# Kernel optimization log

Measured on AMD Instinct MI355X. Metric: run time of the kernel, lower is better.

The kernel has to match this reference:

```python
import jax, jax.numpy as jnp
import numpy as np
from jax import lax

B, S, F, D, H, L, A = 16, 512, 64, 512, 8, 4, 3
E = D // H  # head_dim = 64

def _gelu(t):
    return jax.nn.gelu(t, approximate=False)  # torch nn.GELU() is exact erf

def _make_masks():
    i = jnp.arange(S)[:, None]
    j = jnp.arange(S)[None, :]
    d = jnp.abs(i - j)
    ms = []
    for h in range(min(5, H)):
        dil = 2 ** h
        ms.append((d <= dil) | (d % (2 ** (h + 1)) == 0))
    m = jnp.stack(ms)  # [5,S,S] bool
    idx = jnp.minimum(jnp.arange(H), m.shape[0] - 1)
    return m[idx]  # [H,S,S]

MASKS = _make_masks()

def _ln(x, g, b, eps=1e-5):
    mu = jnp.mean(x, -1, keepdims=True)
    var = jnp.mean((x - mu) ** 2, -1, keepdims=True)
    return (x - mu) * lax.rsqrt(var + eps) * g + b

def _conv1d(x_ncw, w, b):
    y = lax.conv_general_dilated(x_ncw, w, (1,), [(1, 1)],
                                 dimension_numbers=("NCH", "OIH", "NCH"))
    return y + b[None, :, None]

def _attn(x, Wq, bq, Wk, bk, Wv, bv, Wo, bo):
    # x: [B,S,D]; Wq/Wk/Wv: [H,E,D] (stacked per-head Linear weights)
    q = jnp.einsum("bsd,hed->bhse", x, Wq) + bq[None, :, None, :]
    k = jnp.einsum("bsd,hed->bhse", x, Wk) + bk[None, :, None, :]
    v = jnp.einsum("bsd,hed->bhse", x, Wv) + bv[None, :, None, :]
    s = jnp.einsum("bhse,bhte->bhst", q, k) / (E ** 0.5)
    s = jnp.where(MASKS[None], s, -jnp.inf)  # log-sparse masked_fill
    p = jax.nn.softmax(s, axis=-1)
    o = jnp.einsum("bhst,bhte->bhse", p, v)
    o = o.transpose(0, 2, 1, 3).reshape(x.shape[0], x.shape[1], D)  # concat heads
    return o @ Wo.T + bo

def _forward(x, conv1_w, conv1_b, conv2_w, conv2_b, emb_w, emb_b, pos,
             Wq, bq, Wk, bk, Wv, bv, Wo, bo, ln1_g, ln1_b, ln2_g, ln2_b,
             W1, b1, W2, b2, lnf_g, lnf_b,
             a1_w, a1_b, a2_w, a2_b, a3_w, a3_b, a4_w, a4_b,
             c1_w, c1_b, c2_w, c2_b, c3_w, c3_b, c4_w, c4_b):
    # feature extractor: two conv1d+GELU over time axis
    h0 = _gelu(_conv1d(x.transpose(0, 2, 1), conv1_w, conv1_b))
    h0 = _gelu(_conv1d(h0, conv2_w, conv2_b)).transpose(0, 2, 1)  # [B,S,D]
    z = h0 @ emb_w.T + emb_b + pos[:, :S]  # input embedding + positional
    for l in range(L):  # PyraFormer blocks (pre-norm residual)
        z = z + _attn(_ln(z, ln1_g[l], ln1_b[l]),
                      Wq[l], bq[l], Wk[l], bk[l], Wv[l], bv[l], Wo[l], bo[l])
        h = _ln(z, ln2_g[l], ln2_b[l])
        z = z + (_gelu(h @ W1[l].T + b1[l]) @ W2[l].T + b2[l])
    z = _ln(z, lnf_g, lnf_b)
    feat = z[:, -1, :]  # last timestep features

    def head(f, layers):
        (w1, bb1), (w2, bb2), (w3, bb3), (w4, bb4) = layers
        f = _gelu(f @ w1.T + bb1)
        f = _gelu(f @ w2.T + bb2)
        f = _gelu(f @ w3.T + bb3)
        return f @ w4.T + bb4

    policy = head(feat, [(a1_w, a1_b), (a2_w, a2_b), (a3_w, a3_b), (a4_w, a4_b)])
    value = head(feat, [(c1_w, c1_b), (c2_w, c2_b), (c3_w, c3_b), (c4_w, c4_b)])
    return policy, value

def setup_inputs() -> dict:
    key = jax.random.key(0)
    ks = iter(jax.random.split(key, 64))
    r = lambda shape, s=0.05: jax.random.normal(next(ks), shape, jnp.float32) * s
    return {
        "x": jax.random.normal(next(ks), (B, S, F), jnp.float32),
        "conv1_w": r((D // 2, F, 3)), "conv1_b": jnp.zeros((D // 2,)),
        "conv2_w": r((D, D // 2, 3)), "conv2_b": jnp.zeros((D,)),
        "emb_w": r((D, D)), "emb_b": jnp.zeros((D,)),
        "pos": r((1, S, D), 0.02),
        "Wq": r((L, H, E, D)), "bq": jnp.zeros((L, H, E)),
        "Wk": r((L, H, E, D)), "bk": jnp.zeros((L, H, E)),
        "Wv": r((L, H, E, D)), "bv": jnp.zeros((L, H, E)),
        "Wo": r((L, D, D)), "bo": jnp.zeros((L, D)),
        "ln1_g": jnp.ones((L, D)), "ln1_b": jnp.zeros((L, D)),
        "ln2_g": jnp.ones((L, D)), "ln2_b": jnp.zeros((L, D)),
        "W1": r((L, 4 * D, D)), "b1": jnp.zeros((L, 4 * D)),
        "W2": r((L, D, 4 * D)), "b2": jnp.zeros((L, D)),
        "lnf_g": jnp.ones((D,)), "lnf_b": jnp.zeros((D,)),
        "a1_w": r((128, D)), "a1_b": jnp.zeros((128,)),
        "a2_w": r((256, 128)), "a2_b": jnp.zeros((256,)),
        "a3_w": r((57, 256)), "a3_b": jnp.zeros((57,)),
        "a4_w": r((A, 57)), "a4_b": jnp.zeros((A,)),
        "c1_w": r((128, D)), "c1_b": jnp.zeros((128,)),
        "c2_w": r((256, 128)), "c2_b": jnp.zeros((256,)),
        "c3_w": r((57, 256)), "c3_b": jnp.zeros((57,)),
        "c4_w": r((1, 57)), "c4_b": jnp.zeros((1,)),
    }

def reference(x, conv1_w, conv1_b, conv2_w, conv2_b, emb_w, emb_b, pos,
              Wq, bq, Wk, bk, Wv, bv, Wo, bo, ln1_g, ln1_b, ln2_g, ln2_b,
              W1, b1, W2, b2, lnf_g, lnf_b,
              a1_w, a1_b, a2_w, a2_b, a3_w, a3_b, a4_w, a4_b,
              c1_w, c1_b, c2_w, c2_b, c3_w, c3_b, c4_w, c4_b):
    return _forward(x, conv1_w, conv1_b, conv2_w, conv2_b, emb_w, emb_b, pos,
                    Wq, bq, Wk, bk, Wv, bv, Wo, bo, ln1_g, ln1_b, ln2_g, ln2_b,
                    W1, b1, W2, b2, lnf_g, lnf_b,
                    a1_w, a1_b, a2_w, a2_b, a3_w, a3_b, a4_w, a4_b,
                    c1_w, c1_b, c2_w, c2_b, c3_w, c3_b, c4_w, c4_b)
```

## Files before the change

### kernel.cpp

```cpp
#include <hip/hip_runtime.h>
#include <hip/hip_bf16.h>
#include <cstdint>

typedef __attribute__((ext_vector_type(8))) short bf16x8;
typedef __attribute__((ext_vector_type(4))) float f32x4;
typedef unsigned short u16;

#define DEV __device__ __forceinline__

DEV float b2f(u16 u) {
  union { unsigned int i; float f; } v; v.i = ((unsigned int)u) << 16; return v.f;
}
DEV u16 f2b(float f) {
  __hip_bfloat16 h = __float2bfloat16(f);
  return *reinterpret_cast<u16*>(&h);
}
DEV float erf_fast(float x) {
  float ax = fabsf(x);
  float t = __builtin_amdgcn_rcpf(fmaf(0.3275911f, ax, 1.0f));
  float p = t * fmaf(t, fmaf(t, fmaf(t, fmaf(t, 1.061405429f, -1.453152027f),
                                     1.421413741f), -0.284496736f), 0.254829592f);
  float r = fmaf(-p, __expf(-ax * ax), 1.0f);
  return copysignf(r, x);
}
DEV float gelu_f(float x) { return 0.5f * x * (1.0f + erf_fast(x * 0.70710678118654752f)); }

DEV void async_cp16(const u16* g, u16* l) {
  __builtin_amdgcn_global_load_lds(
      (const __attribute__((address_space(1))) void*)g,
      (__attribute__((address_space(3))) void*)l, 16, 0, 0);
}

__global__ void probe_kernel(const unsigned int* __restrict__ g, int* __restrict__ flag) {
  if (threadIdx.x == 0 && blockIdx.x == 0) *flag = (*g == 0x3F800000u) ? 1 : 0;
}

struct CvtArgs {
  const void* src[42];
  unsigned int off[43];
};

struct alignas(16) U8v { u16 u[8]; };
struct alignas(8)  U4v { u16 u[4]; };

__global__ __launch_bounds__(256) void cvt_kernel(CvtArgs a, int n_t, unsigned int total,
                                                  const int* __restrict__ flag,
                                                  u16* __restrict__ dst) {
  unsigned int i8 = (blockIdx.x * 256u + threadIdx.x) * 8u;
  if (i8 >= total) return;
  int t = 0;
  while (t + 1 < n_t && i8 >= a.off[t + 1]) t++;
  unsigned int j = i8 - a.off[t];
  bool in_seg = (i8 + 8 <= a.off[t + 1]) && (i8 + 8 <= total);
  int fp32 = *flag;
  if (fp32) {
    if (in_seg && ((j & 3) == 0)) {
      const float* s = (const float*)a.src[t] + j;
      float4 v0 = *(const float4*)s;
      float4 v1 = *(const float4*)(s + 4);
      U8v o;
      o.u[0] = f2b(v0.x); o.u[1] = f2b(v0.y); o.u[2] = f2b(v0.z); o.u[3] = f2b(v0.w);
      o.u[4] = f2b(v1.x); o.u[5] = f2b(v1.y); o.u[6] = f2b(v1.z); o.u[7] = f2b(v1.w);
      *(U8v*)(dst + i8) = o;
    } else {
      for (int k = 0; k < 8; k++) {
        unsigned int i = i8 + k;
        if (i >= total) break;
        int tt = t;
        while (tt + 1 < n_t && i >= a.off[tt + 1]) tt++;
        dst[i] = f2b(((const float*)a.src[tt])[i - a.off[tt]]);
      }
    }
  } else {
    if (in_seg && ((j & 7) == 0)) {
      *(U8v*)(dst + i8) = *(const U8v*)((const u16*)a.src[t] + j);
    } else {
      for (int k = 0; k < 8; k++) {
        unsigned int i = i8 + k;
        if (i >= total) break;
        int tt = t;
        while (tt + 1 < n_t && i >= a.off[tt + 1]) tt++;
        dst[i] = ((const u16*)a.src[tt])[i - a.off[tt]];
      }
    }
  }
}

__global__ __launch_bounds__(256) void gemm_bt44(
    const u16* __restrict__ A, const u16* __restrict__ W,
    const u16* __restrict__ bias,
    u16* __restrict__ outB, float* __restrict__ outF,
    int N, int K, int mode)
{
  __shared__ __align__(16) u16 As[2][64 * 32];
  __shared__ __align__(16) u16 Bs[2][64 * 32];
  int t = threadIdx.x, l = t & 63, w = t >> 6;
  int wr = w >> 1, wc = w & 1;
  int col = l & 15, quad = l >> 4;
  int q8 = (quad ^ ((col >> 1) & 3)) * 8;
  int m0 = blockIdx.x * 64;
  int n0 = blockIdx.y * 64;

  f32x4 acc[2][2];
#pragma unroll
  for (int i = 0; i < 2; i++)
#pragma unroll
    for (int j = 0; j < 2; j++) acc[i][j] = (f32x4){0.f, 0.f, 0.f, 0.f};

  int ra = t >> 2;
  int ca = (t & 3) ^ ((ra >> 1) & 3);
  const u16* a1 = A + (size_t)(m0 + ra) * K + ca * 8;
  const u16* b1 = W + (size_t)(n0 + ra) * K + ca * 8;

  int nK = K >> 5;
  async_cp16(a1, &As[0][t * 8]);
  async_cp16(b1, &Bs[0][t * 8]);
  for (int ki = 0; ki < nK; ki++) {
    int cur = ki & 1;
    if (ki + 1 < nK) {
      int nxt = cur ^ 1, kt = (ki + 1) << 5;
      async_cp16(a1 + kt, &As[nxt][t * 8]);
      async_cp16(b1 + kt, &Bs[nxt][t * 8]);
      __builtin_amdgcn_s_waitcnt(0x0F72);
    } else {
      __builtin_amdgcn_s_waitcnt(0x0F70);
    }
    __builtin_amdgcn_s_barrier();
    __builtin_amdgcn_sched_barrier(0);
    bf16x8 af[2], bfv[2];
#pragma unroll
    for (int mi = 0; mi < 2; mi++)
      af[mi] = *(const bf16x8*)&As[cur][(wr * 32 + mi * 16 + col) * 32 + q8];
#pragma unroll
    for (int ni = 0; ni < 2; ni++)
      bfv[ni] = *(const bf16x8*)&Bs[cur][(wc * 32 + ni * 16 + col) * 32 + q8];
#pragma unroll
    for (int mi = 0; mi < 2; mi++)
#pragma unroll
      for (int ni = 0; ni < 2; ni++)
        acc[mi][ni] = __builtin_amdgcn_mfma_f32_16x16x32_bf16(bfv[ni], af[mi], acc[mi][ni], 0, 0, 0);
    __builtin_amdgcn_sched_barrier(0);
    __builtin_amdgcn_s_barrier();
  }

  int mBase = m0 + wr * 32, nBase = n0 + wc * 32;
  if (mode == 1) {
#pragma unroll
    for (int mi = 0; mi < 2; mi++) {
      int m = mBase + mi * 16 + col;
      size_t rowOff = (size_t)m * N;
#pragma unroll
      for (int ni = 0; ni < 2; ni++) {
        int n4 = nBase + ni * 16 + quad * 4;
        U4v bb = *(const U4v*)&bias[n4];
        f32x4 v = acc[mi][ni];
        U4v o;
#pragma unroll
        for (int r = 0; r < 4; r++) o.u[r] = f2b(gelu_f(v[r] + b2f(bb.u[r])));
        *(U4v*)&outB[rowOff + n4] = o;
      }
    }
  } else {
#pragma unroll
    for (int mi = 0; mi < 2; mi++) {
      int m = mBase + mi * 16 + col;
      size_t rowOff = (size_t)m * N;
#pragma unroll
      for (int ni = 0; ni < 2; ni++) {
        int n4 = nBase + ni * 16 + quad * 4;
        U4v bb = *(const U4v*)&bias[n4];
        f32x4 v = acc[mi][ni];
        float4* p = (float4*)&outF[rowOff + n4];
        float4 zv = *p;
        zv.x += v[0] + b2f(bb.u[0]);
        zv.y += v[1] + b2f(bb.u[1]);
        zv.z += v[2] + b2f(bb.u[2]);
        zv.w += v[3] + b2f(bb.u[3]);
        *p = zv;
      }
    }
  }
}

__global__ __launch_bounds__(256) void gemm_qkv64(
    const u16* __restrict__ A,
    const u16* __restrict__ Wq, const u16* __restrict__ Wk, const u16* __restrict__ Wv,
    const u16* __restrict__ bq, const u16* __restrict__ bk, const u16* __restrict__ bv,
    u16* __restrict__ outQ, u16* __restrict__ outK, u16* __restrict__ outVT, int K)
{
  __shared__ __align__(16) u16 As[2][64 * 32];
  __shared__ __align__(16) u16 Bs[2][128 * 32];
  int t = threadIdx.x, l = t & 63, w = t >> 6;
  int wr = w >> 1, wc = w & 1;
  int col = l & 15, quad = l >> 4;
  int q8 = (quad ^ ((col >> 1) & 3)) * 8;
  int m0 = blockIdx.x * 64;
  int sel = blockIdx.y >> 2;
  int n0 = (blockIdx.y & 3) * 128;
  const u16* W = sel == 0 ? Wq : (sel == 1 ? Wk : Wv);
  const u16* bias = sel == 0 ? bq : (sel == 1 ? bk : bv);
  const bool swp = (sel < 2);
  const float scl = sel == 0 ? 0.125f : 1.0f;

  f32x4 acc[2][4];
#pragma unroll
  for (int i = 0; i < 2; i++)
#pragma unroll
    for (int j = 0; j < 4; j++) acc[i][j] = (f32x4){0.f, 0.f, 0.f, 0.f};

  int ra = t >> 2;
  int ca = (t & 3) ^ ((ra >> 1) & 3);
  int g1i = t, g2i = t + 256;
  int rb1 = g1i >> 2, rb2 = g2i >> 2;
  int cb1 = (g1i & 3) ^ ((rb1 >> 1) & 3);
  int cb2 = (g2i & 3) ^ ((rb2 >> 1) & 3);
  const u16* a1 = A + (size_t)(m0 + ra) * K + ca * 8;
  const u16* b1 = W + (size_t)(n0 + rb1) * K + cb1 * 8;
  const u16* b2 = W + (size_t)(n0 + rb2) * K + cb2 * 8;

  int nK = K >> 5;
  async_cp16(a1, &As[0][t * 8]);
  async_cp16(b1, &Bs[0][g1i * 8]);
  async_cp16(b2, &Bs[0][g2i * 8]);
  for (int ki = 0; ki < nK; ki++) {
    int cur = ki & 1;
    if (ki + 1 < nK) {
      int nxt = cur ^ 1, kt = (ki + 1) << 5;
      async_cp16(a1 + kt, &As[nxt][t * 8]);
      async_cp16(b1 + kt, &Bs[nxt][g1i * 8]);
      async_cp16(b2 + kt, &Bs[nxt][g2i * 8]);
      __builtin_amdgcn_s_waitcnt(0x0F73);
    } else {
      __builtin_amdgcn_s_waitcnt(0x0F70);
    }
    __builtin_amdgcn_s_barrier();
    __builtin_amdgcn_sched_barrier(0);
    bf16x8 af[2], bfv[4];
#pragma unroll
    for (int mi = 0; mi < 2; mi++)
      af[mi] = *(const bf16x8*)&As[cur][(wr * 32 + mi * 16 + col) * 32 + q8];
#pragma unroll
    for (int ni = 0; ni < 4; ni++)
      bfv[ni] = *(const bf16x8*)&Bs[cur][(wc * 64 + ni * 16 + col) * 32 + q8];
    if (swp) {
#pragma unroll
      for (int mi = 0; mi < 2; mi++)
#pragma unroll
        for (int ni = 0; ni < 4; ni++)
          acc[mi][ni] = __builtin_amdgcn_mfma_f32_16x16x32_bf16(bfv[ni], af[mi], acc[mi][ni], 0, 0, 0);
    } else {
#pragma unroll
      for (int mi = 0; mi < 2; mi++)
#pragma unroll
        for (int ni = 0; ni < 4; ni++)
          acc[mi][ni] = __builtin_amdgcn_mfma_f32_16x16x32_bf16(af[mi], bfv[ni], acc[mi][ni], 0, 0, 0);
    }
    __builtin_amdgcn_sched_barrier(0);
    __builtin_amdgcn_s_barrier();
  }

  int mBase = m0 + wr * 32, nBase = n0 + wc * 64;
  if (swp) {
    u16* outB = sel == 0 ? outQ : outK;
#pragma unroll
    for (int mi = 0; mi < 2; mi++) {
      int m = mBase + mi * 16 + col;
      size_t rowOff = (size_t)m * 512;
#pragma unroll
      for (int ni = 0; ni < 4; ni++) {
        int n4 = nBase + ni * 16 + quad * 4;
        U4v bb = *(const U4v*)&bias[n4];
        f32x4 v = acc[mi][ni];
        U4v o;
#pragma unroll
        for (int r = 0; r < 4; r++) o.u[r] = f2b((v[r] + b2f(bb.u[r])) * scl);
        *(U4v*)&outB[rowOff + n4] = o;
      }
    }
  } else {
    int b = m0 >> 9;
    int sB = m0 & 511;
#pragma unroll
    for (int mi = 0; mi < 2; mi++) {
      int s4 = sB + wr * 32 + mi * 16 + quad * 4;
#pragma unroll
      for (int ni = 0; ni < 4; ni++) {
        int n = nBase + ni * 16 + col;
        int h = n >> 6, e = n & 63;
        float bvv = b2f(bias[n]);
        f32x4 v = acc[mi][ni];
        U4v o;
#pragma unroll
        for (int r = 0; r < 4; r++) o.u[r] = f2b(v[r] + bvv);
        *(U4v*)&outVT[((size_t)((b * 8 + h) * 64 + e)) * 512 + s4] = o;
      }
    }
  }
}

__global__ __launch_bounds__(256) void zinit_kernel(const u16* __restrict__ pos,
                                                    float* __restrict__ z)
{
  int i = (blockIdx.x * 256 + threadIdx.x) * 8;
  int n = i & 511;
  int m = i >> 9;
  int s = m & 511;
  U8v p = *(const U8v*)&pos[s * 512 + n];
  float4 o0 = {b2f(p.u[0]), b2f(p.u[1]), b2f(p.u[2]), b2f(p.u[3])};
  float4 o1 = {b2f(p.u[4]), b2f(p.u[5]), b2f(p.u[6]), b2f(p.u[7])};
  *(float4*)(z + i) = o0;
  *(float4*)(z + i + 4) = o1;
}

__global__ void im2col3_kernel(const u16* __restrict__ src,
                               u16* __restrict__ dst, int C)
{
  int m = blockIdx.x;
  int k = blockIdx.y * blockDim.x + threadIdx.x;
  int ci = k / 3;
  int tap = k - ci * 3;
  int s = m & 511;
  int sp = s + tap - 1;
  u16 val = 0;
  if (sp >= 0 && sp < 512) val = src[(size_t)(m + tap - 1) * C + ci];
  dst[(size_t)m * (3 * C) + k] = val;
}

__global__ __launch_bounds__(256) void ln_kernel(
    const float* __restrict__ z, const u16* __restrict__ gam,
    const u16* __restrict__ bet, u16* __restrict__ out)
{
  int w = threadIdx.x >> 6, l = threadIdx.x & 63;
  int row = blockIdx.x * 4 + w;
  const float* zr = z + (size_t)row * 512;
  float4 v0 = *(const float4*)(zr + l * 8);
  float4 v1 = *(const float4*)(zr + l * 8 + 4);
  float x[8] = {v0.x, v0.y, v0.z, v0.w, v1.x, v1.y, v1.z, v1.w};
  float s = 0.f;
#pragma unroll
  for (int i = 0; i < 8; i++) s += x[i];
#pragma unroll
  for (int mm = 1; mm < 64; mm <<= 1) s += __shfl_xor(s, mm, 64);
  float mu = s * (1.0f / 512.0f);
  float vs = 0.f;
#pragma unroll
  for (int i = 0; i < 8; i++) { float d = x[i] - mu; vs += d * d; }
#pragma unroll
  for (int mm = 1; mm < 64; mm <<= 1) vs += __shfl_xor(vs, mm, 64);
  float rs = rsqrtf(vs * (1.0f / 512.0f) + 1e-5f);
  U8v gg = *(const U8v*)(gam + l * 8);
  U8v bb = *(const U8v*)(bet + l * 8);
  U8v o;
#pragma unroll
  for (int i = 0; i < 8; i++) o.u[i] = f2b((x[i] - mu) * rs * b2f(gg.u[i]) + b2f(bb.u[i]));
  *(U8v*)(out + (size_t)row * 512 + l * 8) = o;
}

__global__ __launch_bounds__(256) void lnf_kernel(
    const float* __restrict__ z, const u16* __restrict__ gam,
    const u16* __restrict__ bet, u16* __restrict__ feat)
{
  int w = threadIdx.x >> 6, l = threadIdx.x & 63;
  int b = blockIdx.x * 4 + w;
  const float* zr = z + ((size_t)b * 512 + 511) * 512;
  float4 v0 = *(const float4*)(zr + l * 8);
  float4 v1 = *(const float4*)(zr + l * 8 + 4);
  float x[8] = {v0.x, v0.y, v0.z, v0.w, v1.x, v1.y, v1.z, v1.w};
  float s = 0.f;
#pragma unroll
  for (int i = 0; i < 8; i++) s += x[i];
#pragma unroll
  for (int mm = 1; mm < 64; mm <<= 1) s += __shfl_xor(s, mm, 64);
  float mu = s * (1.0f / 512.0f);
  float vs = 0.f;
#pragma unroll
  for (int i = 0; i < 8; i++) { float d = x[i] - mu; vs += d * d; }
#pragma unroll
  for (int mm = 1; mm < 64; mm <<= 1) vs += __shfl_xor(vs, mm, 64);
  float rs = rsqrtf(vs * (1.0f / 512.0f) + 1e-5f);
  U8v gg = *(const U8v*)(gam + l * 8);
  U8v bb = *(const U8v*)(bet + l * 8);
  U8v o;
#pragma unroll
  for (int i = 0; i < 8; i++) o.u[i] = f2b((x[i] - mu) * rs * b2f(gg.u[i]) + b2f(bb.u[i]));
  *(U8v*)(feat + (size_t)b * 512 + l * 8) = o;
}

#define AST 72
__global__ __launch_bounds__(256) void attn_kernel(
    const u16* __restrict__ Q, const u16* __restrict__ Kg,
    const u16* __restrict__ VT, u16* __restrict__ O)
{
  __shared__ __align__(16) u16 Ks[64 * AST];
  __shared__ __align__(16) u16 Vts[64 * AST];
  __shared__ __align__(16) u16 Ps[64 * AST];
  const float NEG = -1e30f;
  int blk = blockIdx.x;
  int bh = blk & 127;
  int i0 = (blk >> 7) * 64;
  int b = bh >> 3, h = bh & 7;
  int t = threadIdx.x, w = t >> 6, l = t & 63;
  int col = l & 15, quad = l >> 4;
  int dil = 1 << (h < 4 ? h : 4);
  int per_m1 = 2 * dil - 1;

  {
    int row = t >> 2, c = (t & 3) * 16;
    const u16* src = Q + ((size_t)(b * 512 + i0 + row) * 512 + h * 64 + c);
    *(float4*)&Ps[row * AST + c] = *(const float4*)src;
    *(float4*)&Ps[row * AST + c + 8] = *(const float4*)(src + 8);
  }
  __builtin_amdgcn_s_waitcnt(0xC07F);
  __builtin_amdgcn_sched_barrier(0);
  bf16x8 qa[2];
#pragma unroll
  for (int kk = 0; kk < 2; kk++)
    qa[kk] = *(const bf16x8*)&Ps[(w * 16 + col) * AST + kk * 32 + quad * 8];

  f32x4 acc_o[4];
#pragma unroll
  for (int i = 0; i < 4; i++) acc_o[i] = (f32x4){0.f, 0.f, 0.f, 0.f};
  float m_run = NEG, l_run = 0.f;
  int ig = i0 + w * 16 + col;

  for (int jt = 0; jt < 8; jt++) {
    int j0 = jt * 64;
    {
      int row = t >> 2, c = (t & 3) * 16;
      const u16* ks = Kg + ((size_t)(b * 512 + j0 + row) * 512 + h * 64 + c);
      *(float4*)&Ks[row * AST + c] = *(const float4*)ks;
      *(float4*)&Ks[row * AST + c + 8] = *(const float4*)(ks + 8);
      const u16* vs = VT + ((size_t)(bh * 64 + row) * 512 + j0 + c);
      *(float4*)&Vts[row * AST + c] = *(const float4*)vs;
      *(float4*)&Vts[row * AST + c + 8] = *(const float4*)(vs + 8);
    }
    __syncthreads();

    f32x4 sa[4];
    __builtin_amdgcn_s_setprio(1);
#pragma unroll
    for (int ni = 0; ni < 4; ni++) {
      f32x4 s = (f32x4){0.f, 0.f, 0.f, 0.f};
#pragma unroll
      for (int kk = 0; kk < 2; kk++) {
        bf16x8 kb = *(const bf16x8*)&Ks[(ni * 16 + col) * AST + kk * 32 + quad * 8];
        s = __builtin_amdgcn_mfma_f32_16x16x32_bf16(kb, qa[kk], s, 0, 0, 0);
      }
      sa[ni] = s;
    }
    __builtin_amdgcn_s_setprio(0);

    float mx = NEG;
#pragma unroll
    for (int ni = 0; ni < 4; ni++)
#pragma unroll
      for (int r = 0; r < 4; r++) {
        int jg = j0 + ni * 16 + quad * 4 + r;
        int d = ig - jg; d = d < 0 ? -d : d;
        bool keep = (d <= dil) || ((d & per_m1) == 0);
        float s = keep ? sa[ni][r] : NEG;
        sa[ni][r] = s;
        mx = fmaxf(mx, s);
      }
    mx = fmaxf(mx, __shfl_xor(mx, 16, 64));
    mx = fmaxf(mx, __shfl_xor(mx, 32, 64));
    float mN = fmaxf(m_run, mx);
    float alpha = __expf(m_run - mN);
    m_run = mN;
    float rsum = 0.f;
#pragma unroll
    for (int ni = 0; ni < 4; ni++)
#pragma unroll
      for (int r = 0; r < 4; r++) {
        float p = __expf(sa[ni][r] - mN);
        sa[ni][r] = p;
        rsum += p;
      }
    rsum += __shfl_xor(rsum, 16, 64);
    rsum += __shfl_xor(rsum, 32, 64);
    l_run = l_run * alpha + rsum;

#pragma unroll
    for (int ni = 0; ni < 4; ni++) {
      unsigned int lo = (unsigned int)f2b(sa[ni][0]) | ((unsigned int)f2b(sa[ni][1]) << 16);
      unsigned int hi = (unsigned int)f2b(sa[ni][2]) | ((unsigned int)f2b(sa[ni][3]) << 16);
      uint2 pk; pk.x = lo; pk.y = hi;
      *(uint2*)&Ps[(w * 16 + col) * AST + ni * 16 + quad * 4] = pk;
    }
    __builtin_amdgcn_s_waitcnt(0xC07F);
    __builtin_amdgcn_sched_barrier(0);

    float a_sh[4];
#pragma unroll
    for (int r = 0; r < 4; r++) a_sh[r] = __shfl(alpha, quad * 4 + r, 64);
#pragma unroll
    for (int ne = 0; ne < 4; ne++)
#pragma unroll
      for (int r = 0; r < 4; r++) acc_o[ne][r] *= a_sh[r];

    bf16x8 pa[2];
#pragma unroll
    for (int kk = 0; kk < 2; kk++)
      pa[kk] = *(const bf16x8*)&Ps[(w * 16 + col) * AST + kk * 32 + quad * 8];
    __builtin_amdgcn_s_setprio(1);
#pragma unroll
    for (int ne = 0; ne < 4; ne++) {
#pragma unroll
      for (int kk = 0; kk < 2; kk++) {
        bf16x8 vb = *(const bf16x8*)&Vts[(ne * 16 + col) * AST + kk * 32 + quad * 8];
        acc_o[ne] = __builtin_amdgcn_mfma_f32_16x16x32_bf16(pa[kk], vb, acc_o[ne], 0, 0, 0);
      }
    }
    __builtin_amdgcn_s_setprio(0);
    __syncthreads();
  }

  float inv[4];
#pragma unroll
  for (int r = 0; r < 4; r++) {
    float lr = __shfl(l_run, quad * 4 + r, 64);
    inv[r] = 1.0f / fmaxf(lr, 1e-20f);
  }
#pragma unroll
  for (int ne = 0; ne < 4; ne++)
#pragma unroll
    for (int r = 0; r < 4; r++) {
      float o = acc_o[ne][r] * inv[r];
      O[((size_t)(b * 512 + i0 + w * 16 + quad * 4 + r)) * 512 + h * 64 + ne * 16 + col] = f2b(o);
    }
}

__global__ __launch_bounds__(256) void heads_kernel(
    const u16* __restrict__ feat,
    const u16* __restrict__ a1w, const u16* __restrict__ a1b,
    const u16* __restrict__ a2w, const u16* __restrict__ a2b,
    const u16* __restrict__ a3w, const u16* __restrict__ a3b,
    const u16* __restrict__ a4w, const u16* __restrict__ a4b,
    const u16* __restrict__ c1w, const u16* __restrict__ c1b,
    const u16* __restrict__ c2w, const u16* __restrict__ c2b,
    const u16* __restrict__ c3w, const u16* __restrict__ c3b,
    const u16* __restrict__ c4w, const u16* __restrict__ c4b,
    const int* __restrict__ flag, void* __restrict__ outv)
{
  __shared__ float f[512];
  __shared__ float g1[256];
  __shared__ float g2[512];
  __shared__ float g3[128];
  int b = blockIdx.x, t = threadIdx.x;
  f[t] = b2f(feat[b * 512 + t]);
  f[t + 256] = b2f(feat[b * 512 + 256 + t]);
  __syncthreads();
  {
    const u16* wrow; float bias;
    if (t < 128) { wrow = a1w + (size_t)t * 512; bias = b2f(a1b[t]); }
    else { wrow = c1w + (size_t)(t - 128) * 512; bias = b2f(c1b[t - 128]); }
    float s = bias;
    for (int k = 0; k < 512; k++) s += b2f(wrow[k]) * f[k];
    g1[t] = gelu_f(s);
  }
  __syncthreads();
  {
    float s1 = b2f(a2b[t]);
    for (int k = 0; k < 128; k++) s1 += b2f(a2w[t * 128 + k]) * g1[k];
    float s2 = b2f(c2b[t]);
    for (int k = 0; k < 128; k++) s2 += b2f(c2w[t * 128 + k]) * g1[128 + k];
    g2[t] = gelu_f(s1);
    g2[256 + t] = gelu_f(s2);
  }
  __syncthreads();
  if (t < 57) {
    float s = b2f(a3b[t]);
    for (int k = 0; k < 256; k++) s += b2f(a3w[t * 256 + k]) * g2[k];
    g3[t] = gelu_f(s);
  } else if (t >= 64 && t < 121) {
    int u = t - 64;
    float s = b2f(c3b[u]);
    for (int k = 0; k < 256; k++) s += b2f(c3w[u * 256 + k]) * g2[256 + k];
    g3[64 + u] = gelu_f(s);
  }
  __syncthreads();
  int fp32out = *flag;
  if (t < 3) {
    float s = b2f(a4b[t]);
    for (int k = 0; k < 57; k++) s += b2f(a4w[t * 57 + k]) * g3[k];
    if (fp32out) ((float*)outv)[b * 3 + t] = s;
    else ((u16*)outv)[b * 3 + t] = f2b(s);
  } else if (t == 4) {
    float s = b2f(c4b[0]);
    for (int k = 0; k < 57; k++) s += b2f(c4w[k]) * g3[64 + k];
    if (fp32out) ((float*)outv)[48 + b] = s;
    else ((u16*)outv)[48 + b] = f2b(s);
  }
}

extern "C" void kernel_launch(void* const* d_in, const int* in_sizes, int n_in,
                              void* d_out, int out_size, void* d_ws, size_t ws_size,
                              hipStream_t stream)
{
  char* ws = (char*)d_ws;
  float* z    = (float*)ws;
  u16* R      = (u16*)(ws + (16u << 20));
  u16* bufQ   = R;
  u16* bufK   = (u16*)(ws + (24u << 20));
  u16* bufO   = (u16*)(ws + (32u << 20));
  u16* bufVT  = (u16*)(ws + (40u << 20));
  u16* bufH   = (u16*)(ws + (48u << 20));
  u16* feat   = R;
  u16* pool   = (u16*)(ws + (56u << 20));
  int* flag   = (int*)(ws + (88u << 20));

  CvtArgs args;
  unsigned int off = 0;
  int nt = n_in < 42 ? n_in : 42;
  for (int i = 0; i < nt; i++) { args.src[i] = d_in[i]; args.off[i] = off; off += (unsigned int)in_sizes[i]; }
  args.off[nt] = off;
  unsigned int total = off;

  probe_kernel<<<1, 64, 0, stream>>>((const unsigned int*)d_in[24], flag);
  cvt_kernel<<<(total + 2047) / 2048, 256, 0, stream>>>(args, nt, total, flag, pool);

  const u16* P[42];
  for (int i = 0; i < nt; i++) P[i] = pool + args.off[i];
  const u16* x       = P[0];
  const u16* conv1_w = P[1];  const u16* conv1_b = P[2];
  const u16* conv2_w = P[3];  const u16* conv2_b = P[4];
  const u16* emb_w   = P[5];  const u16* emb_b   = P[6];
  const u16* pos     = P[7];
  const u16* Wq      = P[8];  const u16* bq      = P[9];
  const u16* Wk      = P[10]; const u16* bk      = P[11];
  const u16* Wv      = P[12]; const u16* bv      = P[13];
  const u16* Wo      = P[14]; const u16* bo      = P[15];
  const u16* ln1_g   = P[16]; const u16* ln1_b   = P[17];
  const u16* ln2_g   = P[18]; const u16* ln2_b   = P[19];
  const u16* W1      = P[20]; const u16* b1      = P[21];
  const u16* W2      = P[22]; const u16* b2      = P[23];
  const u16* lnf_g   = P[24]; const u16* lnf_b   = P[25];

  im2col3_kernel<<<dim3(8192, 1), 192, 0, stream>>>(x, R, 64);
  gemm_bt44<<<dim3(128, 4), 256, 0, stream>>>(R, conv1_w, conv1_b, bufH, nullptr, 256, 192, 1);
  im2col3_kernel<<<dim3(8192, 3), 256, 0, stream>>>(bufH, R, 256);
  gemm_bt44<<<dim3(128, 8), 256, 0, stream>>>(R, conv2_w, conv2_b, bufH, nullptr, 512, 768, 1);
  zinit_kernel<<<2048, 256, 0, stream>>>(pos, z);
  gemm_bt44<<<dim3(128, 8), 256, 0, stream>>>(bufH, emb_w, emb_b, nullptr, z, 512, 512, 2);

  for (int l = 0; l < 4; l++) {
    ln_kernel<<<2048, 256, 0, stream>>>(z, ln1_g + l * 512, ln1_b + l * 512, bufH);
    gemm_qkv64<<<dim3(128, 12), 256, 0, stream>>>(bufH,
        Wq + (size_t)l * 262144, Wk + (size_t)l * 262144, Wv + (size_t)l * 262144,
        bq + l * 512, bk + l * 512, bv + l * 512, bufQ, bufK, bufVT, 512);
    attn_kernel<<<dim3(1024), 256, 0, stream>>>(bufQ, bufK, bufVT, bufO);
    gemm_bt44<<<dim3(128, 8), 256, 0, stream>>>(bufO, Wo + (size_t)l * 262144, bo + l * 512, nullptr, z, 512, 512, 2);
    ln_kernel<<<2048, 256, 0, stream>>>(z, ln2_g + l * 512, ln2_b + l * 512, bufH);
    gemm_bt44<<<dim3(128, 32), 256, 0, stream>>>(bufH, W1 + (size_t)l * 1048576, b1 + l * 2048, R, nullptr, 2048, 512, 1);
    gemm_bt44<<<dim3(128, 8), 256, 0, stream>>>(R, W2 + (size_t)l * 1048576, b2 + l * 512, nullptr, z, 512, 2048, 2);
  }

  lnf_kernel<<<4, 256, 0, stream>>>(z, lnf_g, lnf_b, feat);
  heads_kernel<<<16, 256, 0, stream>>>(feat,
      P[26], P[27], P[28], P[29], P[30], P[31], P[32], P[33],
      P[34], P[35], P[36], P[37], P[38], P[39], P[40], P[41],
      flag, d_out);
}
```

Baseline: 902.2 us.

## Triple-buffer GEMM shared-memory tiles and drop trailing barrier per K step

Both GEMM kernels move from double-buffered to triple-buffered LDS tiles, so loads are issued two K-steps ahead, right after the barrier. Because the buffer being refilled is never the one being read, the second barrier at the end of each iteration is removed. This aims to hide global load latency and cut synchronisation. In exchange it uses 1.5x the shared memory, which may reduce occupancy, and the waitcnt values now count more loads in flight, so they need to match the deeper prefetch.

```diff
diff --git a/kernel.cpp b/kernel.cpp
--- a/kernel.cpp
+++ b/kernel.cpp
@@ -92,8 +92,8 @@
     u16* __restrict__ outB, float* __restrict__ outF,
     int N, int K, int mode)
 {
-  __shared__ __align__(16) u16 As[2][64 * 32];
-  __shared__ __align__(16) u16 Bs[2][64 * 32];
+  __shared__ __align__(16) u16 As[3][64 * 32];
+  __shared__ __align__(16) u16 Bs[3][64 * 32];
   int t = threadIdx.x, l = t & 63, w = t >> 6;
   int wr = w >> 1, wc = w & 1;
   int col = l & 15, quad = l >> 4;
@@ -115,18 +115,23 @@
   int nK = K >> 5;
   async_cp16(a1, &As[0][t * 8]);
   async_cp16(b1, &Bs[0][t * 8]);
+  async_cp16(a1 + 32, &As[1][t * 8]);
+  async_cp16(b1 + 32, &Bs[1][t * 8]);
+  int cur = 0;
   for (int ki = 0; ki < nK; ki++) {
-    int cur = ki & 1;
     if (ki + 1 < nK) {
-      int nxt = cur ^ 1, kt = (ki + 1) << 5;
-      async_cp16(a1 + kt, &As[nxt][t * 8]);
-      async_cp16(b1 + kt, &Bs[nxt][t * 8]);
       __builtin_amdgcn_s_waitcnt(0x0F72);
     } else {
       __builtin_amdgcn_s_waitcnt(0x0F70);
     }
     __builtin_amdgcn_s_barrier();
     __builtin_amdgcn_sched_barrier(0);
+    if (ki + 2 < nK) {
+      int sb = cur == 0 ? 2 : cur - 1;
+      int kt = (ki + 2) << 5;
+      async_cp16(a1 + kt, &As[sb][t * 8]);
+      async_cp16(b1 + kt, &Bs[sb][t * 8]);
+    }
     bf16x8 af[2], bfv[2];
 #pragma unroll
     for (int mi = 0; mi < 2; mi++)
@@ -140,7 +145,7 @@
       for (int ni = 0; ni < 2; ni++)
         acc[mi][ni] = __builtin_amdgcn_mfma_f32_16x16x32_bf16(bfv[ni], af[mi], acc[mi][ni], 0, 0, 0);
     __builtin_amdgcn_sched_barrier(0);
-    __builtin_amdgcn_s_barrier();
+    cur = cur == 2 ? 0 : cur + 1;
   }
 
   int mBase = m0 + wr * 32, nBase = n0 + wc * 32;
@@ -188,8 +193,8 @@
     const u16* __restrict__ bq, const u16* __restrict__ bk, const u16* __restrict__ bv,
     u16* __restrict__ outQ, u16* __restrict__ outK, u16* __restrict__ outVT, int K)
 {
-  __shared__ __align__(16) u16 As[2][64 * 32];
-  __shared__ __align__(16) u16 Bs[2][128 * 32];
+  __shared__ __align__(16) u16 As[3][64 * 32];
+  __shared__ __align__(16) u16 Bs[3][128 * 32];
   int t = threadIdx.x, l = t & 63, w = t >> 6;
   int wr = w >> 1, wc = w & 1;
   int col = l & 15, quad = l >> 4;
@@ -222,19 +227,25 @@
   async_cp16(a1, &As[0][t * 8]);
   async_cp16(b1, &Bs[0][g1i * 8]);
   async_cp16(b2, &Bs[0][g2i * 8]);
+  async_cp16(a1 + 32, &As[1][t * 8]);
+  async_cp16(b1 + 32, &Bs[1][g1i * 8]);
+  async_cp16(b2 + 32, &Bs[1][g2i * 8]);
+  int cur = 0;
   for (int ki = 0; ki < nK; ki++) {
-    int cur = ki & 1;
     if (ki + 1 < nK) {
-      int nxt = cur ^ 1, kt = (ki + 1) << 5;
-      async_cp16(a1 + kt, &As[nxt][t * 8]);
-      async_cp16(b1 + kt, &Bs[nxt][g1i * 8]);
-      async_cp16(b2 + kt, &Bs[nxt][g2i * 8]);
       __builtin_amdgcn_s_waitcnt(0x0F73);
     } else {
       __builtin_amdgcn_s_waitcnt(0x0F70);
     }
     __builtin_amdgcn_s_barrier();
     __builtin_amdgcn_sched_barrier(0);
+    if (ki + 2 < nK) {
+      int sb = cur == 0 ? 2 : cur - 1;
+      int kt = (ki + 2) << 5;
+      async_cp16(a1 + kt, &As[sb][t * 8]);
+      async_cp16(b1 + kt, &Bs[sb][g1i * 8]);
+      async_cp16(b2 + kt, &Bs[sb][g2i * 8]);
+    }
     bf16x8 af[2], bfv[4];
 #pragma unroll
     for (int mi = 0; mi < 2; mi++)
@@ -256,7 +267,7 @@
           acc[mi][ni] = __builtin_amdgcn_mfma_f32_16x16x32_bf16(af[mi], bfv[ni], acc[mi][ni], 0, 0, 0);
     }
     __builtin_amdgcn_sched_barrier(0);
-    __builtin_amdgcn_s_barrier();
+    cur = cur == 2 ? 0 : cur + 1;
   }
 
   int mBase = m0 + wr * 32, nBase = n0 + wc * 64;
```

After: 917.6 us. About the same (+1.7%).
